# Optimization experiments

Measured on AMD Instinct MI355X. Metric: run time of the kernel, lower is better.

Reference implementation:

```python
import jax, jax.numpy as jnp
import numpy as np
from jax import lax

B, C, H, W = 2, 256, 64, 64
KC, RD = C // 8, C // 16  # key_channels=32, GatherExcite rd_channels=16
EPS = 1e-5


def setup_inputs() -> dict:
    key = jax.random.key(0)
    ks = jax.random.split(key, 17)
    s = 0.05
    n = lambda k, shp: jax.random.normal(k, shp, jnp.float32) * s
    return {
        "x": jax.random.normal(ks[0], (B, C, H, W), jnp.float32),
        "Wq": n(ks[1], (KC, C)),
        "Wk": n(ks[2], (KC, C)),
        "Wv": n(ks[3], (C, C)),
        "Wb1": n(ks[4], (KC, C)),
        "Wb2": n(ks[5], (KC, C)),
        "w_gb": jax.random.normal(ks[6], (), jnp.float32),  # 1x1 conv on 1-channel bias map
        "ge_w1": n(ks[7], (RD, C)),
        "ge_b1": jnp.zeros((RD,), jnp.float32),
        "ge_w2": n(ks[8], (C, RD)),
        "ge_b2": jnp.zeros((C,), jnp.float32),
        "Wo": n(ks[9], (C, C)),
        "bn_scale": jnp.ones((C,), jnp.float32),
        "bn_bias": jnp.zeros((C,), jnp.float32),
        "bn_mean": jax.random.normal(ks[10], (C,), jnp.float32) * 0.01,
        "bn_var": jnp.ones((C,), jnp.float32),
        "gamma": jax.random.normal(ks[11], (), jnp.float32) * 0.1,
    }


def _conv1x1(t, w):  # t: [B,Cin,H,W], w: [Cout,Cin]
    return jnp.einsum('bchw,oc->bohw', t, w)


def reference(x, Wq, Wk, Wv, Wb1, Wb2, w_gb, ge_w1, ge_b1, ge_w2, ge_b2,
              Wo, bn_scale, bn_bias, bn_mean, bn_var, gamma):
    b, c, h, w = x.shape
    hw = h * w

    # GatherExcite (extent=0, use_mlp=True, gate=sigmoid): global mean -> ConvMlp -> sigmoid gate
    m = x.mean(axis=(2, 3), keepdims=True)                     # [B,C,1,1]
    g = jax.nn.relu(_conv1x1(m, ge_w1) + ge_b1[None, :, None, None])
    g = _conv1x1(g, ge_w2) + ge_b2[None, :, None, None]
    key_in = x * jax.nn.sigmoid(g)                             # [B,C,H,W]

    value = _conv1x1(x, Wv).reshape(b, c, hw).transpose(0, 2, 1)   # [B,HW,C]
    query = _conv1x1(x, Wq).reshape(b, KC, hw).transpose(0, 2, 1)  # [B,HW,Kc]
    key_f = _conv1x1(key_in, Wk).reshape(b, KC, hw)                # [B,Kc,HW]

    sim = jnp.einsum('bnk,bkm->bnm', query, key_f)                 # [B,HW,HW]

    # bias branch (dropout is identity at eval)
    b1 = jax.nn.relu(_conv1x1(x, Wb1)).reshape(b, KC, hw)          # [B,Kc,HW]
    b2 = jax.nn.relu(_conv1x1(x, Wb2)).reshape(b, KC, hw)          # [B,Kc,HW]
    bias = jnp.einsum('bkn,bkm->bnm', b1, b2)                      # [B,HW,HW]

    # AvgPool2d(k=3, s=1, pad=1, count_include_pad=True) on [B,1,HW,HW]
    pooled = lax.reduce_window(bias[:, None], 0.0, lax.add,
                               (1, 1, 3, 3), (1, 1, 1, 1),
                               [(0, 0), (0, 0), (1, 1), (1, 1)]) / 9.0
    bias_map = jax.nn.sigmoid(w_gb * pooled)[:, 0]                 # [B,HW,HW]

    attn = jax.nn.softmax(sim * bias_map, axis=-1)                 # [B,HW,HW]
    ctx = jnp.einsum('bnm,bmc->bnc', attn, value)                  # [B,HW,C]
    ctx = ctx.transpose(0, 2, 1).reshape(b, c, h, w)

    # W: conv1x1 -> BatchNorm (inference) -> ReLU
    y = _conv1x1(ctx, Wo)
    y = (y - bn_mean[None, :, None, None]) * (bn_scale / jnp.sqrt(bn_var + EPS))[None, :, None, None] \
        + bn_bias[None, :, None, None]
    y = jax.nn.relu(y)

    return gamma * y + x
```

## Files before the change

kernel.cpp:

```cpp
#include <hip/hip_runtime.h>
#include <hip/hip_bf16.h>

typedef __bf16 bf16;
typedef __bf16 v8bf __attribute__((ext_vector_type(8)));
typedef __bf16 v4bf __attribute__((ext_vector_type(4)));
typedef float v4f __attribute__((ext_vector_type(4)));

#define HW 4096
#define CH 256
#define KC 32
#define RD 16
#define NB 2
#define BNEPS 1e-5f
#define LOG2E 1.4426950408889634f

__device__ __forceinline__ float fexp2(float x) {
#if __has_builtin(__builtin_amdgcn_exp2f)
  return __builtin_amdgcn_exp2f(x);
#else
  return exp2f(x);
#endif
}
__device__ __forceinline__ float frcp(float x) {
#if __has_builtin(__builtin_amdgcn_rcpf)
  return __builtin_amdgcn_rcpf(x);
#else
  return 1.f / x;
#endif
}

__device__ __forceinline__ int xcd_swz(int bid, int nwg) {
  return (bid & 7) * (nwg >> 3) + (bid >> 3);
}

#define OFF_QT     0u
#define OFF_KT     524288u
#define OFF_BS1    1048576u
#define OFF_BS2    1572864u
#define OFF_VF     2097152u
#define OFF_B1R    6291456u
#define OFF_B2R    6815744u
#define OFF_PACC   7340032u
#define OFF_PL     40894464u
#define OFF_WOBF   41156608u
#define OFF_XBT    41287680u
#define OFF_WALL   45481984u
#define OFF_MPART  45875200u

__global__ __launch_bounds__(256) void k_prep(const float* __restrict__ x,
    bf16* __restrict__ xbt, float* __restrict__ mpart) {
  __shared__ __align__(16) float ts[64][68];
  const int blk = blockIdx.x;
  const int b  = blk >> 8;
  const int id = blk & 255;
  const int ct = id >> 6, nt = id & 63;
  const int c0 = ct * 64, n0 = nt * 64;
  const int t = threadIdx.x;
  const int crow = t >> 2, nch = (t & 3) * 16;
  const float* xp = x + ((size_t)(b * CH + c0 + crow)) * HW + n0 + nch;
  #pragma unroll
  for (int i = 0; i < 4; ++i)
    *(v4f*)&ts[crow][nch + i * 4] = *(const v4f*)(xp + i * 4);
  __syncthreads();
  {
    float p = 0.f;
    #pragma unroll
    for (int j = 0; j < 16; ++j) p += ts[crow][nch + j];
    p += __shfl_xor(p, 1);
    p += __shfl_xor(p, 2);
    if ((t & 3) == 0) mpart[(size_t)(b * CH + c0 + crow) * 64 + nt] = p;
  }
  const int nl = t >> 2, cc0 = (t & 3) * 16;
  bf16* dst = xbt + ((size_t)(b * HW + n0 + nl)) * CH + c0 + cc0;
  v8bf o0, o1;
  #pragma unroll
  for (int j = 0; j < 8; ++j) { o0[j] = (bf16)ts[cc0 + j][nl]; o1[j] = (bf16)ts[cc0 + 8 + j][nl]; }
  *(v8bf*)dst = o0;
  *(v8bf*)(dst + 8) = o1;
}

__global__ __launch_bounds__(256) void k_pack(
    const float* __restrict__ mpart,
    const float* __restrict__ gw1, const float* __restrict__ gb1,
    const float* __restrict__ gw2, const float* __restrict__ gb2,
    const float* __restrict__ Wq, const float* __restrict__ Wk,
    const float* __restrict__ Wb1, const float* __restrict__ Wb2,
    const float* __restrict__ Wv, const float* __restrict__ Wo,
    bf16* __restrict__ wall, bf16* __restrict__ wo_bf) {
  __shared__ float ms[CH];
  __shared__ float hid[RD];
  const int blk = blockIdx.x;
  const int t = threadIdx.x;
  if (blk >= 768) {
    int i = (blk - 768) * 256 + t;
    wo_bf[i] = (bf16)Wo[i];
    return;
  }
  const int b = blk / 384, row = blk % 384;
  float v;
  if (row < 32)       v = Wq[row * CH + t] * LOG2E;
  else if (row < 64) {
    float m = 0.f;
    const float* mp = mpart + (size_t)(b * CH + t) * 64;
    #pragma unroll
    for (int j = 0; j < 64; ++j) m += mp[j];
    ms[t] = m * (1.0f / HW);
    __syncthreads();
    if (t < RD) {
      float a = gb1[t];
      for (int c = 0; c < CH; ++c) a += gw1[t * CH + c] * ms[c];
      hid[t] = fmaxf(a, 0.f);
    }
    __syncthreads();
    float a = gb2[t];
    #pragma unroll
    for (int r = 0; r < RD; ++r) a += gw2[t * RD + r] * hid[r];
    float s = 1.f / (1.f + __expf(-a));
    v = Wk[(row - 32) * CH + t] * s;
  }
  else if (row < 96)  v = Wb1[(row - 64) * CH + t];
  else if (row < 128) v = Wb2[(row - 96) * CH + t];
  else                v = Wv[(row - 128) * CH + t];
  wall[((size_t)b * 384 + row) * CH + t] = (bf16)v;
}

__global__ __launch_bounds__(256, 4) void k_proj(
    const bf16* __restrict__ xbt, const bf16* __restrict__ wall,
    bf16* __restrict__ qt, bf16* __restrict__ kt,
    bf16* __restrict__ b1r, bf16* __restrict__ b2r, bf16* __restrict__ vfg) {
  __shared__ __align__(16) bf16 xs[16][264];
  __shared__ __align__(16) bf16 tr[4][16][24];
  const int blk = blockIdx.x;
  const int b = blk >> 8, nt = blk & 255;
  const int n0 = nt * 16;
  const int t = threadIdx.x;
  {
    const int row = t >> 4, c0 = (t & 15) * 16;
    const bf16* src = xbt + ((size_t)(b * HW + n0 + row)) * CH + c0;
    *(v8bf*)&xs[row][c0] = *(const v8bf*)src;
    *(v8bf*)&xs[row][c0 + 8] = *(const v8bf*)(src + 8);
  }
  __syncthreads();
  const int w = t >> 6, lane = t & 63, cl = lane & 15, kh = lane >> 4;
  const v4f vzero = {0.f, 0.f, 0.f, 0.f};
  v4f acc[6] = {vzero, vzero, vzero, vzero, vzero, vzero};
  const bf16* wb = wall + ((size_t)b * 384 + w * 96) * CH;
  for (int kk = 0; kk < 8; ++kk) {
    v8bf bx = *(const v8bf*)&xs[cl][kk * 32 + kh * 8];
    #pragma unroll
    for (int j = 0; j < 6; ++j) {
      v8bf af = *(const v8bf*)(wb + (size_t)(j * 16 + cl) * CH + kk * 32 + kh * 8);
      acc[j] = __builtin_amdgcn_mfma_f32_16x16x32_bf16(af, bx, acc[j], 0, 0, 0);
    }
  }
  const int n = n0 + cl;
  #pragma unroll
  for (int j = 0; j < 6; ++j) {
    const int o0 = w * 96 + j * 16;
    if (o0 < 128) {
      const bool rel = (o0 >= 64);
      v4bf pk;
      #pragma unroll
      for (int r = 0; r < 4; ++r) {
        float v = acc[j][r];
        if (rel) v = fmaxf(v, 0.f);
        pk[r] = (bf16)v;
      }
      const int seg = o0 >> 5;
      bf16* base = seg == 0 ? qt : seg == 1 ? kt : seg == 2 ? b1r : b2r;
      *(v4bf*)&base[((size_t)b * HW + n) * KC + (o0 & 31) + kh * 4] = pk;
    } else {
      #pragma unroll
      for (int r = 0; r < 4; ++r) tr[w][kh * 4 + r][cl] = (bf16)acc[j][r];
      asm volatile("s_waitcnt lgkmcnt(0)" ::: "memory");
      __builtin_amdgcn_sched_barrier(0);
      if (lane < 32) {
        const int clf = lane & 15, khl = (lane >> 4) & 1;
        const int khf = (((n0 >> 4) & 1) << 1) + khl;
        const int s = n0 >> 5, f = (o0 - 128) >> 4;
        v8bf d = *(const v8bf*)&tr[w][clf][khl * 8];
        *(v8bf*)&vfg[((((size_t)b * 128 + s) * 16 + f) * 64 + khf * 16 + clf) * 8] = d;
      }
    }
  }
}

__global__ __launch_bounds__(256) void k_pool(const bf16* __restrict__ b1r,
    const bf16* __restrict__ b2r, const float* __restrict__ wgb,
    bf16* __restrict__ bs1, bf16* __restrict__ bs2) {
  int i = blockIdx.x * 256 + threadIdx.x;
  int n = (i >> 5) & (HW - 1);
  float a = (float)b1r[i], c = (float)b2r[i];
  if (n > 0)      { a += (float)b1r[i - KC]; c += (float)b2r[i - KC]; }
  if (n < HW - 1) { a += (float)b1r[i + KC]; c += (float)b2r[i + KC]; }
  const float ws = -LOG2E * wgb[0] * (1.f / 9.f);
  bs1[i] = (bf16)(a * ws);
  bs2[i] = (bf16)c;
}

__global__ __launch_bounds__(256, 4) void k_attn(
    const bf16* __restrict__ qtg, const bf16* __restrict__ ktg,
    const bf16* __restrict__ bs1g, const bf16* __restrict__ bs2g,
    const bf16* __restrict__ vfg,
    bf16* __restrict__ pacc, float* __restrict__ pl) {
  __shared__ __align__(16) bf16 kbuf[2][32][40];
  __shared__ __align__(16) bf16 bbuf[2][32][40];
  __shared__ __align__(16) bf16 plds[2][64][40];
  __shared__ __align__(16) bf16 escr[4][16][72];
  const int blk = xcd_swz(blockIdx.x, 1024);
  const int rt  = blk >> 3;
  const int os  = blk & 7;
  const int b   = rt >> 6;
  const int row0 = (rt & 63) * 64;
  const int t = threadIdx.x;
  const int w = t >> 6;
  const int lane = t & 63;
  const int cl = lane & 15, kh = lane >> 4;
  const int kb = os * 512;
  const v4f vzero = {0.f, 0.f, 0.f, 0.f};
  const size_t qoff = ((size_t)(b * HW + row0 + w * 16 + cl)) * KC + kh * 8;
  const v8bf qf  = *(const v8bf*)(qtg + qoff);
  const v8bf b1f = *(const v8bf*)(bs1g + qoff);
  const bf16* kt = ktg + (size_t)b * HW * KC;
  const bf16* b2 = bs2g + (size_t)b * HW * KC;
  const bf16* vfb = vfg + ((((size_t)b * 128 + (kb >> 5)) * 16) + w * 4) * 512 + (size_t)lane * 8;
  const int sr = (t >> 2) & 31, sl = (t & 3) * 8;
  const bf16* sbase = (t < 128) ? kt : b2;
  bf16* sd0 = (t < 128) ? &kbuf[0][sr][sl] : &bbuf[0][sr][sl];
  bf16* sd1 = (t < 128) ? &kbuf[1][sr][sl] : &bbuf[1][sr][sl];

  *(v8bf*)sd0 = *(const v8bf*)(sbase + (size_t)(kb + sr) * KC + sl);
  __syncthreads();

  v4f acc[16];
  #pragma unroll
  for (int f = 0; f < 16; ++f) acc[f] = vzero;
  float psum = 0.f;

  for (int s = 0; s < 16; ++s) {
    const int m0 = kb + s * 32;
    const int pb = s & 1;
    const bf16* vs = vfb + (size_t)s * 8192;
    v8bf vf0 = *(const v8bf*)(vs);
    v8bf vf1 = *(const v8bf*)(vs + 512);
    v8bf vf2 = *(const v8bf*)(vs + 1024);
    v8bf vf3 = *(const v8bf*)(vs + 1536);
    v8bf pr;
    if (s < 15)
      pr = *(const v8bf*)(sbase + (size_t)(m0 + 32 + sr) * KC + sl);
    #pragma unroll
    for (int cb = 0; cb < 2; ++cb) {
      v8bf kf  = *(const v8bf*)&kbuf[pb][cb * 16 + cl][kh * 8];
      v8bf b2f = *(const v8bf*)&bbuf[pb][cb * 16 + cl][kh * 8];
      v4f sim = __builtin_amdgcn_mfma_f32_16x16x32_bf16(kf,  qf,  vzero, 0, 0, 0);
      v4f bia = __builtin_amdgcn_mfma_f32_16x16x32_bf16(b2f, b1f, vzero, 0, 0, 0);
      v4bf pk;
      #pragma unroll
      for (int r = 0; r < 4; ++r) {
        float bm = frcp(1.f + fexp2(bia[r]));
        float pv = fexp2(sim[r] * bm);
        psum += pv;
        pk[r] = (bf16)pv;
      }
      *(v4bf*)&plds[pb][w * 16 + cl][cb * 16 + kh * 4] = pk;
    }
    if (s < 15) {
      bf16* sd = pb ? sd0 : sd1;
      *(v8bf*)sd = pr;
    }
    __syncthreads();
    __builtin_amdgcn_s_setprio(1);
    #pragma unroll
    for (int rg = 0; rg < 4; ++rg) {
      v8bf pa = *(const v8bf*)&plds[pb][rg * 16 + cl][kh * 8];
      acc[rg * 4 + 0] = __builtin_amdgcn_mfma_f32_16x16x32_bf16(pa, vf0, acc[rg * 4 + 0], 0, 0, 0);
      acc[rg * 4 + 1] = __builtin_amdgcn_mfma_f32_16x16x32_bf16(pa, vf1, acc[rg * 4 + 1], 0, 0, 0);
      acc[rg * 4 + 2] = __builtin_amdgcn_mfma_f32_16x16x32_bf16(pa, vf2, acc[rg * 4 + 2], 0, 0, 0);
      acc[rg * 4 + 3] = __builtin_amdgcn_mfma_f32_16x16x32_bf16(pa, vf3, acc[rg * 4 + 3], 0, 0, 0);
    }
    __builtin_amdgcn_s_setprio(0);
  }
  __syncthreads();

  {
    float s2 = psum;
    s2 += __shfl_xor(s2, 16);
    s2 += __shfl_xor(s2, 32);
    if (kh == 0) pl[blk * 64 + w * 16 + cl] = s2;
  }
  bf16* po = pacc + (size_t)blk * 64 * CH;
  for (int rg = 0; rg < 4; ++rg) {
    #pragma unroll
    for (int f = 0; f < 4; ++f)
      #pragma unroll
      for (int r = 0; r < 4; ++r)
        escr[w][kh * 4 + r][f * 16 + cl] = (bf16)acc[rg * 4 + f][r];
    asm volatile("s_waitcnt lgkmcnt(0)" ::: "memory");
    __builtin_amdgcn_sched_barrier(0);
    #pragma unroll
    for (int it = 0; it < 2; ++it) {
      int row = lane >> 2, chunk = it * 4 + (lane & 3);
      v8bf d = *(const v8bf*)&escr[w][row][chunk * 8];
      *(v8bf*)&po[(size_t)(rg * 16 + row) * CH + w * 64 + chunk * 8] = d;
    }
  }
}

__global__ __launch_bounds__(256) void k_outc(
    const bf16* __restrict__ pacc, const float* __restrict__ pl,
    const bf16* __restrict__ wo,
    const float* __restrict__ bns, const float* __restrict__ bnb,
    const float* __restrict__ bnm, const float* __restrict__ bnv,
    const float* __restrict__ gamma, const float* __restrict__ x,
    float* __restrict__ out) {
  __shared__ __align__(16) bf16 cs[16][264];
  const int blk = xcd_swz(blockIdx.x, 512);
  const int n0g = blk * 16;
  const int b   = n0g >> 12;
  const int n0  = n0g & (HW - 1);
  const int t = threadIdx.x;
  const int base = (blk >> 2) * 8;
  {
    const int r16 = t >> 4;
    const int ch0 = (t & 15) * 16;
    const int rl = (blk & 3) * 16 + r16;
    float den = 0.f;
    #pragma unroll
    for (int s = 0; s < 8; ++s) den += pl[(base + s) * 64 + rl];
    const float inv = 1.f / den;
    float sum[16];
    #pragma unroll
    for (int j = 0; j < 16; ++j) sum[j] = 0.f;
    #pragma unroll
    for (int s = 0; s < 8; ++s) {
      const bf16* pp = &pacc[((size_t)(base + s) * 64 + rl) * CH + ch0];
      v8bf p0 = *(const v8bf*)pp;
      v8bf p1 = *(const v8bf*)(pp + 8);
      #pragma unroll
      for (int j = 0; j < 8; ++j) { sum[j] += (float)p0[j]; sum[8 + j] += (float)p1[j]; }
    }
    v8bf o0, o1;
    #pragma unroll
    for (int j = 0; j < 8; ++j) {
      o0[j] = (bf16)(sum[j] * inv);
      o1[j] = (bf16)(sum[8 + j] * inv);
    }
    *(v8bf*)&cs[r16][ch0] = o0;
    *(v8bf*)&cs[r16][ch0 + 8] = o1;
  }
  __syncthreads();
  const int w = t >> 6, lane = t & 63, cl = lane & 15, kh = lane >> 4;
  const v4f vzero = {0.f, 0.f, 0.f, 0.f};
  v8bf a[8];
  #pragma unroll
  for (int kk = 0; kk < 8; ++kk)
    a[kk] = *(const v8bf*)&cs[cl][kk * 32 + kh * 8];
  v4f acc[4] = {vzero, vzero, vzero, vzero};
  #pragma unroll
  for (int kk = 0; kk < 8; ++kk)
    #pragma unroll
    for (int cg = 0; cg < 4; ++cg) {
      v8bf bfr = *(const v8bf*)(wo + (size_t)(w * 64 + cg * 16 + cl) * CH + kk * 32 + kh * 8);
      acc[cg] = __builtin_amdgcn_mfma_f32_16x16x32_bf16(a[kk], bfr, acc[cg], 0, 0, 0);
    }
  const float g = gamma[0];
  #pragma unroll
  for (int cg = 0; cg < 4; ++cg) {
    int o = w * 64 + cg * 16 + cl;
    float isc = bns[o] / sqrtf(bnv[o] + BNEPS);
    float mu = bnm[o], bb = bnb[o];
    size_t oi = ((size_t)b * CH + o) * HW + n0 + kh * 4;
    v4f xv = *(const v4f*)&x[oi];
    v4f ov;
    #pragma unroll
    for (int r = 0; r < 4; ++r) {
      float v = (acc[cg][r] - mu) * isc + bb;
      v = fmaxf(v, 0.f);
      ov[r] = g * v + xv[r];
    }
    *(v4f*)&out[oi] = ov;
  }
}

extern "C" void kernel_launch(void* const* d_in, const int* in_sizes, int n_in,
                              void* d_out, int out_size, void* d_ws, size_t ws_size,
                              hipStream_t stream) {
  const float* x    = (const float*)d_in[0];
  const float* Wq   = (const float*)d_in[1];
  const float* Wk   = (const float*)d_in[2];
  const float* Wv   = (const float*)d_in[3];
  const float* Wb1  = (const float*)d_in[4];
  const float* Wb2  = (const float*)d_in[5];
  const float* wgb  = (const float*)d_in[6];
  const float* gw1  = (const float*)d_in[7];
  const float* gb1  = (const float*)d_in[8];
  const float* gw2  = (const float*)d_in[9];
  const float* gb2  = (const float*)d_in[10];
  const float* Wo   = (const float*)d_in[11];
  const float* bns  = (const float*)d_in[12];
  const float* bnb  = (const float*)d_in[13];
  const float* bnm  = (const float*)d_in[14];
  const float* bnv  = (const float*)d_in[15];
  const float* gam  = (const float*)d_in[16];

  char* ws = (char*)d_ws;
  bf16* qt    = (bf16*)(ws + OFF_QT);
  bf16* kt    = (bf16*)(ws + OFF_KT);
  bf16* bs1   = (bf16*)(ws + OFF_BS1);
  bf16* bs2   = (bf16*)(ws + OFF_BS2);
  bf16* vfg   = (bf16*)(ws + OFF_VF);
  bf16* b1r   = (bf16*)(ws + OFF_B1R);
  bf16* b2r   = (bf16*)(ws + OFF_B2R);
  bf16* pacc  = (bf16*)(ws + OFF_PACC);
  float* plv  = (float*)(ws + OFF_PL);
  bf16* wobf  = (bf16*)(ws + OFF_WOBF);
  bf16* xbt   = (bf16*)(ws + OFF_XBT);
  bf16* wall  = (bf16*)(ws + OFF_WALL);
  float* mprt = (float*)(ws + OFF_MPART);
  float* out  = (float*)d_out;

  hipLaunchKernelGGL(k_prep, dim3(512),  dim3(256), 0, stream, x, xbt, mprt);
  hipLaunchKernelGGL(k_pack, dim3(1024), dim3(256), 0, stream, mprt, gw1, gb1, gw2, gb2,
                     Wq, Wk, Wb1, Wb2, Wv, Wo, wall, wobf);
  hipLaunchKernelGGL(k_proj, dim3(512),  dim3(256), 0, stream, xbt, wall, qt, kt, b1r, b2r, vfg);
  hipLaunchKernelGGL(k_pool, dim3(NB * HW * KC / 256), dim3(256), 0, stream, b1r, b2r, wgb, bs1, bs2);
  hipLaunchKernelGGL(k_attn, dim3(1024), dim3(256), 0, stream, qt, kt, bs1, bs2, vfg, pacc, plv);
  hipLaunchKernelGGL(k_outc, dim3(512),  dim3(256), 0, stream, pacc, plv, wobf, bns, bnb, bnm, bnv, gam, x, out);
}
```

Before: 79.37 us.

## Fold bias pooling into projection and attention kernels, drop k_pool launch

Removes the separate k_pool kernel. The scale factor is applied to b1 inside k_proj, and the 3-tap neighbour sums for b1 and b2 are computed on the fly inside k_attn when it loads query rows and stages key tiles. This saves a kernel launch and one global round-trip of the pooled bias tensors. In exchange, the attention staging path does extra global loads and conversions, and the value-fragment loads move after the barrier, which may expose their latency.

New measurement: 116.6 us. +46.9%, slower.

```diff
diff --git a/kernel.cpp b/kernel.cpp
--- a/kernel.cpp
+++ b/kernel.cpp
@@ -35,11 +35,9 @@
 
 #define OFF_QT     0u
 #define OFF_KT     524288u
-#define OFF_BS1    1048576u
-#define OFF_BS2    1572864u
+#define OFF_B1S    1048576u
+#define OFF_B2R    1572864u
 #define OFF_VF     2097152u
-#define OFF_B1R    6291456u
-#define OFF_B2R    6815744u
 #define OFF_PACC   7340032u
 #define OFF_PL     40894464u
 #define OFF_WOBF   41156608u
@@ -126,8 +124,9 @@
 
 __global__ __launch_bounds__(256, 4) void k_proj(
     const bf16* __restrict__ xbt, const bf16* __restrict__ wall,
+    const float* __restrict__ wgb,
     bf16* __restrict__ qt, bf16* __restrict__ kt,
-    bf16* __restrict__ b1r, bf16* __restrict__ b2r, bf16* __restrict__ vfg) {
+    bf16* __restrict__ b1s, bf16* __restrict__ b2r, bf16* __restrict__ vfg) {
   __shared__ __align__(16) bf16 xs[16][264];
   __shared__ __align__(16) bf16 tr[4][16][24];
   const int blk = blockIdx.x;
@@ -153,21 +152,22 @@
       acc[j] = __builtin_amdgcn_mfma_f32_16x16x32_bf16(af, bx, acc[j], 0, 0, 0);
     }
   }
+  const float ws = -LOG2E * wgb[0] * (1.f / 9.f);
   const int n = n0 + cl;
   #pragma unroll
   for (int j = 0; j < 6; ++j) {
     const int o0 = w * 96 + j * 16;
     if (o0 < 128) {
-      const bool rel = (o0 >= 64);
+      const int seg = o0 >> 5;
       v4bf pk;
       #pragma unroll
       for (int r = 0; r < 4; ++r) {
         float v = acc[j][r];
-        if (rel) v = fmaxf(v, 0.f);
+        if (seg == 2)      v = ws * fmaxf(v, 0.f);
+        else if (seg == 3) v = fmaxf(v, 0.f);
         pk[r] = (bf16)v;
       }
-      const int seg = o0 >> 5;
-      bf16* base = seg == 0 ? qt : seg == 1 ? kt : seg == 2 ? b1r : b2r;
+      bf16* base = seg == 0 ? qt : seg == 1 ? kt : seg == 2 ? b1s : b2r;
       *(v4bf*)&base[((size_t)b * HW + n) * KC + (o0 & 31) + kh * 4] = pk;
     } else {
       #pragma unroll
@@ -185,22 +185,9 @@
   }
 }
 
-__global__ __launch_bounds__(256) void k_pool(const bf16* __restrict__ b1r,
-    const bf16* __restrict__ b2r, const float* __restrict__ wgb,
-    bf16* __restrict__ bs1, bf16* __restrict__ bs2) {
-  int i = blockIdx.x * 256 + threadIdx.x;
-  int n = (i >> 5) & (HW - 1);
-  float a = (float)b1r[i], c = (float)b2r[i];
-  if (n > 0)      { a += (float)b1r[i - KC]; c += (float)b2r[i - KC]; }
-  if (n < HW - 1) { a += (float)b1r[i + KC]; c += (float)b2r[i + KC]; }
-  const float ws = -LOG2E * wgb[0] * (1.f / 9.f);
-  bs1[i] = (bf16)(a * ws);
-  bs2[i] = (bf16)c;
-}
-
 __global__ __launch_bounds__(256, 4) void k_attn(
     const bf16* __restrict__ qtg, const bf16* __restrict__ ktg,
-    const bf16* __restrict__ bs1g, const bf16* __restrict__ bs2g,
+    const bf16* __restrict__ b1sg, const bf16* __restrict__ b2rg,
     const bf16* __restrict__ vfg,
     bf16* __restrict__ pacc, float* __restrict__ pl) {
   __shared__ __align__(16) bf16 kbuf[2][32][40];
@@ -218,18 +205,47 @@
   const int cl = lane & 15, kh = lane >> 4;
   const int kb = os * 512;
   const v4f vzero = {0.f, 0.f, 0.f, 0.f};
-  const size_t qoff = ((size_t)(b * HW + row0 + w * 16 + cl)) * KC + kh * 8;
-  const v8bf qf  = *(const v8bf*)(qtg + qoff);
-  const v8bf b1f = *(const v8bf*)(bs1g + qoff);
   const bf16* kt = ktg + (size_t)b * HW * KC;
-  const bf16* b2 = bs2g + (size_t)b * HW * KC;
+  const bf16* b2 = b2rg + (size_t)b * HW * KC;
+  const int qrow = row0 + w * 16 + cl;
+  const v8bf qf = *(const v8bf*)(qtg + ((size_t)(b * HW + qrow)) * KC + kh * 8);
+  v8bf b1f;
+  {
+    const bf16* bp = b1sg + (size_t)b * HW * KC;
+    v8bf c1 = *(const v8bf*)(bp + (size_t)qrow * KC + kh * 8);
+    v8bf c0 = *(const v8bf*)(bp + (size_t)(qrow > 0 ? qrow - 1 : 0) * KC + kh * 8);
+    v8bf c2 = *(const v8bf*)(bp + (size_t)(qrow < HW - 1 ? qrow + 1 : HW - 1) * KC + kh * 8);
+    #pragma unroll
+    for (int j = 0; j < 8; ++j) {
+      float sv = (float)c1[j];
+      if (qrow > 0)      sv += (float)c0[j];
+      if (qrow < HW - 1) sv += (float)c2[j];
+      b1f[j] = (bf16)sv;
+    }
+  }
   const bf16* vfb = vfg + ((((size_t)b * 128 + (kb >> 5)) * 16) + w * 4) * 512 + (size_t)lane * 8;
   const int sr = (t >> 2) & 31, sl = (t & 3) * 8;
-  const bf16* sbase = (t < 128) ? kt : b2;
-  bf16* sd0 = (t < 128) ? &kbuf[0][sr][sl] : &bbuf[0][sr][sl];
-  bf16* sd1 = (t < 128) ? &kbuf[1][sr][sl] : &bbuf[1][sr][sl];
-
-  *(v8bf*)sd0 = *(const v8bf*)(sbase + (size_t)(kb + sr) * KC + sl);
+  const bool isK = (t < 128);
+  bf16* sd0 = isK ? &kbuf[0][sr][sl] : &bbuf[0][sr][sl];
+  bf16* sd1 = isK ? &kbuf[1][sr][sl] : &bbuf[1][sr][sl];
+
+  if (isK) {
+    *(v8bf*)sd0 = *(const v8bf*)(kt + (size_t)(kb + sr) * KC + sl);
+  } else {
+    const int g = kb + sr;
+    v8bf c1 = *(const v8bf*)(b2 + (size_t)g * KC + sl);
+    v8bf c0 = *(const v8bf*)(b2 + (size_t)(g > 0 ? g - 1 : 0) * KC + sl);
+    v8bf c2 = *(const v8bf*)(b2 + (size_t)(g < HW - 1 ? g + 1 : HW - 1) * KC + sl);
+    v8bf o;
+    #pragma unroll
+    for (int j = 0; j < 8; ++j) {
+      float sv = (float)c1[j];
+      if (g > 0)      sv += (float)c0[j];
+      if (g < HW - 1) sv += (float)c2[j];
+      o[j] = (bf16)sv;
+    }
+    *(v8bf*)sd0 = o;
+  }
   __syncthreads();
 
   v4f acc[16];
@@ -240,14 +256,9 @@
   for (int s = 0; s < 16; ++s) {
     const int m0 = kb + s * 32;
     const int pb = s & 1;
-    const bf16* vs = vfb + (size_t)s * 8192;
-    v8bf vf0 = *(const v8bf*)(vs);
-    v8bf vf1 = *(const v8bf*)(vs + 512);
-    v8bf vf2 = *(const v8bf*)(vs + 1024);
-    v8bf vf3 = *(const v8bf*)(vs + 1536);
     v8bf pr;
     if (s < 15)
-      pr = *(const v8bf*)(sbase + (size_t)(m0 + 32 + sr) * KC + sl);
+      pr = *(const v8bf*)((isK ? kt : b2) + (size_t)(m0 + 32 + sr) * KC + sl);
     #pragma unroll
     for (int cb = 0; cb < 2; ++cb) {
       v8bf kf  = *(const v8bf*)&kbuf[pb][cb * 16 + cl][kh * 8];
@@ -266,9 +277,28 @@
     }
     if (s < 15) {
       bf16* sd = pb ? sd0 : sd1;
-      *(v8bf*)sd = pr;
+      if (isK) {
+        *(v8bf*)sd = pr;
+      } else {
+        const int g = m0 + 32 + sr;
+        v8bf c0 = *(const v8bf*)(b2 + (size_t)(g - 1) * KC + sl);
+        v8bf c2 = *(const v8bf*)(b2 + (size_t)(g < HW - 1 ? g + 1 : HW - 1) * KC + sl);
+        v8bf o;
+        #pragma unroll
+        for (int j = 0; j < 8; ++j) {
+          float sv = (float)pr[j] + (float)c0[j];
+          if (g < HW - 1) sv += (float)c2[j];
+          o[j] = (bf16)sv;
+        }
+        *(v8bf*)sd = o;
+      }
     }
     __syncthreads();
+    const bf16* vs = vfb + (size_t)s * 8192;
+    v8bf vf0 = *(const v8bf*)(vs);
+    v8bf vf1 = *(const v8bf*)(vs + 512);
+    v8bf vf2 = *(const v8bf*)(vs + 1024);
+    v8bf vf3 = *(const v8bf*)(vs + 1536);
     __builtin_amdgcn_s_setprio(1);
     #pragma unroll
     for (int rg = 0; rg < 4; ++rg) {
@@ -406,11 +436,9 @@
   char* ws = (char*)d_ws;
   bf16* qt    = (bf16*)(ws + OFF_QT);
   bf16* kt    = (bf16*)(ws + OFF_KT);
-  bf16* bs1   = (bf16*)(ws + OFF_BS1);
-  bf16* bs2   = (bf16*)(ws + OFF_BS2);
+  bf16* b1s   = (bf16*)(ws + OFF_B1S);
+  bf16* b2r   = (bf16*)(ws + OFF_B2R);
   bf16* vfg   = (bf16*)(ws + OFF_VF);
-  bf16* b1r   = (bf16*)(ws + OFF_B1R);
-  bf16* b2r   = (bf16*)(ws + OFF_B2R);
   bf16* pacc  = (bf16*)(ws + OFF_PACC);
   float* plv  = (float*)(ws + OFF_PL);
   bf16* wobf  = (bf16*)(ws + OFF_WOBF);
@@ -422,8 +450,7 @@
   hipLaunchKernelGGL(k_prep, dim3(512),  dim3(256), 0, stream, x, xbt, mprt);
   hipLaunchKernelGGL(k_pack, dim3(1024), dim3(256), 0, stream, mprt, gw1, gb1, gw2, gb2,
                      Wq, Wk, Wb1, Wb2, Wv, Wo, wall, wobf);
-  hipLaunchKernelGGL(k_proj, dim3(512),  dim3(256), 0, stream, xbt, wall, qt, kt, b1r, b2r, vfg);
-  hipLaunchKernelGGL(k_pool, dim3(NB * HW * KC / 256), dim3(256), 0, stream, b1r, b2r, wgb, bs1, bs2);
-  hipLaunchKernelGGL(k_attn, dim3(1024), dim3(256), 0, stream, qt, kt, bs1, bs2, vfg, pacc, plv);
+  hipLaunchKernelGGL(k_proj, dim3(512),  dim3(256), 0, stream, xbt, wall, wgb, qt, kt, b1s, b2r, vfg);
+  hipLaunchKernelGGL(k_attn, dim3(1024), dim3(256), 0, stream, qt, kt, b1s, b2r, vfg, pacc, plv);
   hipLaunchKernelGGL(k_outc, dim3(512),  dim3(256), 0, stream, pacc, plv, wobf, bns, bnb, bnm, bnv, gam, x, out);
 }
```
